# Performance work log

Measured on AMD Instinct MI355X. Metric: run time of the kernel, lower is better.

The kernel has to match this reference:

```python
import jax, jax.numpy as jnp
import numpy as np

D_MODEL = 1024
N_HEADS = 16
D_HEAD = D_MODEL // N_HEADS
BLOCK = 128
B, T = 2, 2048


def setup_inputs() -> dict:
    key = jax.random.key(0)
    ks = jax.random.split(key, 5)
    x = jax.random.normal(ks[0], (B, T, D_MODEL), dtype=jnp.float32)
    def init_w(k):
        # nn.Linear default init scale ~ 1/sqrt(fan_in)
        return jax.random.normal(k, (D_MODEL, D_MODEL), dtype=jnp.float32) / np.sqrt(D_MODEL).astype(np.float32)
    return {
        "x": x,
        "Wq": init_w(ks[1]),
        "Wk": init_w(ks[2]),
        "Wv": init_w(ks[3]),
        "Wo": init_w(ks[4]),
    }


def _flash_attention(Q, K, V, block_size, scale):
    """Online-softmax tiled attention over kv blocks (causal). Q,K,V: (B,H,T,d)."""
    Bb, H, Tt, d = Q.shape
    n_blocks = Tt // block_size
    # (n_blocks, B, H, block, d) so scan streams kv tiles
    Kb = K.reshape(Bb, H, n_blocks, block_size, d).transpose(2, 0, 1, 3, 4)
    Vb = V.reshape(Bb, H, n_blocks, block_size, d).transpose(2, 0, 1, 3, 4)
    starts = jnp.arange(n_blocks) * block_size
    q_pos = jnp.arange(Tt)

    def step(carry, xs):
        m, l, acc = carry
        kb, vb, st = xs
        # scores: (B,H,T,block)
        scores = scale * jnp.einsum('bhtd,bhsd->bhts', Q, kb)
        kv_pos = st + jnp.arange(block_size)
        future = kv_pos[None, :] > q_pos[:, None]          # (T, block)
        scores = jnp.where(future[None, None], -jnp.inf, scores)
        m_new = jnp.maximum(m, jnp.max(scores, axis=-1, keepdims=True))
        p = jnp.exp(scores - m_new)
        corr = jnp.exp(m - m_new)
        l = corr * l + jnp.sum(p, axis=-1, keepdims=True)
        acc = corr * acc + jnp.einsum('bhts,bhsd->bhtd', p, vb)
        return (m_new, l, acc), None

    m0 = jnp.full((Bb, H, Tt, 1), -jnp.inf, dtype=jnp.float32)
    l0 = jnp.zeros((Bb, H, Tt, 1), dtype=jnp.float32)
    a0 = jnp.zeros((Bb, H, Tt, d), dtype=jnp.float32)
    (m, l, acc), _ = jax.lax.scan(step, (m0, l0, a0), (Kb, Vb, starts))
    return acc / jnp.maximum(l, 1e-12)


def reference(x, Wq, Wk, Wv, Wo):
    Bx, Tx, _ = x.shape
    scale = 1.0 / np.sqrt(D_HEAD).astype(np.float32)
    def proj(W):  # nn.Linear: y = x @ W.T
        y = jnp.einsum('btm,nm->btn', x, W)
        return y.reshape(Bx, Tx, N_HEADS, D_HEAD).transpose(0, 2, 1, 3)
    Q, K, V = proj(Wq), proj(Wk), proj(Wv)
    O = _flash_attention(Q.astype(jnp.float32), K.astype(jnp.float32), V.astype(jnp.float32), BLOCK, scale)
    O = O.astype(x.dtype).transpose(0, 2, 1, 3).reshape(Bx, Tx, D_MODEL)
    return jnp.einsum('btm,nm->btn', O, Wo)
```

## Files before the change

kernel.cpp:

```cpp
#include <hip/hip_runtime.h>
#include <hip/hip_bf16.h>

typedef __attribute__((ext_vector_type(8))) short short8;
typedef __attribute__((ext_vector_type(4))) float f32x4;
typedef __attribute__((ext_vector_type(2))) unsigned int uint2v;
typedef __attribute__((ext_vector_type(4))) unsigned int uint4v;
typedef unsigned short u16;

#define MFMA_BF16(a, b, c) __builtin_amdgcn_mfma_f32_16x16x32_bf16(a, b, c, 0, 0, 0)

#define T_SEQ 2048
#define DMODEL 1024
#define NHEADS 16
#define DHEAD 64
#define NEG_BIG (-30000.0f)
#define QSCALE 0.1803368801111f
#define RESCALE_THR 8.0f

#if __has_builtin(__builtin_amdgcn_exp2f)
#define EXP2(x) __builtin_amdgcn_exp2f(x)
#else
#define EXP2(x) exp2f(x)
#endif

__device__ __forceinline__ unsigned bfr(unsigned u) {
  return (u + 0x7fffu + ((u >> 16) & 1u)) >> 16;
}
__device__ __forceinline__ uint4v ld8bf(const float* __restrict__ p) {
  const uint4v a = *(const uint4v*)p;
  const uint4v b = *(const uint4v*)(p + 4);
  uint4v r;
  r[0] = bfr(a[0]) | (bfr(a[1]) << 16);
  r[1] = bfr(a[2]) | (bfr(a[3]) << 16);
  r[2] = bfr(b[0]) | (bfr(b[1]) << 16);
  r[3] = bfr(b[2]) | (bfr(b[3]) << 16);
  return r;
}
__device__ __forceinline__ u16 f2bf(float f) {
  unsigned u = __float_as_uint(f);
  u += 0x7fffu + ((u >> 16) & 1u);
  return (u16)(u >> 16);
}
__device__ __forceinline__ void gld16(const u16* g, u16* l) {
  __builtin_amdgcn_global_load_lds(
      (const __attribute__((address_space(1))) unsigned int*)g,
      (__attribute__((address_space(3))) unsigned int*)l, 16, 0, 0);
}

__global__ __launch_bounds__(256) void cvt_all(
    const float* __restrict__ x, const float* __restrict__ wq,
    const float* __restrict__ wk, const float* __restrict__ wv,
    const float* __restrict__ wo, u16* __restrict__ xh, u16* __restrict__ wqh,
    u16* __restrict__ wkh, u16* __restrict__ wvh, u16* __restrict__ woh) {
  int bi = blockIdx.x;
  const float* s;
  u16* d;
  size_t base;
  if (bi < 2048) {
    s = x; d = xh; base = (size_t)bi * 2048;
  } else {
    int k = (bi - 2048) >> 9;
    int r = (bi - 2048) & 511;
    s = (k == 0) ? wq : (k == 1) ? wk : (k == 2) ? wv : wo;
    d = (k == 0) ? wqh : (k == 1) ? wkh : (k == 2) ? wvh : woh;
    base = (size_t)r * 2048;
  }
  size_t i = base + (size_t)threadIdx.x * 8;
  *(uint4v*)&d[i] = ld8bf(&s[i]);
}

__global__ __launch_bounds__(256) void gemm_qkv(
    const u16* __restrict__ X, const u16* __restrict__ Wq,
    const u16* __restrict__ Wk, const u16* __restrict__ Wv,
    u16* __restrict__ Qo, u16* __restrict__ Ko, u16* __restrict__ Vo) {
  __shared__ __attribute__((aligned(16))) u16 sm[16384];
  const int tid = threadIdx.x, lane = tid & 63, w = tid >> 6;
  const int wm = (w >> 1) * 64, wn = (w & 1) * 64;
  const int lrow = lane & 15;
  const int lk = (lane >> 4) << 3;
  const int lq = (lane >> 4) << 2;

  const int id = blockIdx.x;
  const int xcd = id & 7, r8 = id >> 3;
  const int xo = r8 & 3, yz = r8 >> 2;
  const int y = yz & 7, z = yz >> 3;
  const int mBase = (xcd * 4 + xo) * 128, nBase = y * 128;

  const u16* Bt = (z == 0) ? Wq : (z == 1) ? Wk : Wv;
  u16* D = (z == 0) ? Qo : (z == 1) ? Ko : Vo;
  const float scale = (z == 0) ? QSCALE : 1.0f;

  f32x4 acc[4][4];
#pragma unroll
  for (int mi = 0; mi < 4; mi++)
#pragma unroll
    for (int ni = 0; ni < 4; ni++) acc[mi][ni] = (f32x4)0.0f;

  auto stage = [&](int buf, int k0) {
#pragma unroll
    for (int i = 0; i < 2; i++) {
      int c = i * 256 + tid;
      int r = c >> 2, kk = (c & 3) << 3;
      gld16(&X[(size_t)(mBase + r) * 1024 + k0 + kk], &sm[buf * 4096 + c * 8]);
      gld16(&Bt[(size_t)(nBase + r) * 1024 + k0 + kk],
            &sm[8192 + buf * 4096 + c * 8]);
    }
  };

  stage(0, 0);
  __syncthreads();
  int cur = 0;
  for (int k0 = 0; k0 < 1024; k0 += 32) {
    if (k0 + 32 < 1024) stage(cur ^ 1, k0 + 32);
    short8 af[4], bf[4];
#pragma unroll
    for (int mi = 0; mi < 4; mi++)
      af[mi] = *(const short8*)&sm[cur * 4096 + (wm + mi * 16 + lrow) * 32 + lk];
#pragma unroll
    for (int ni = 0; ni < 4; ni++)
      bf[ni] =
          *(const short8*)&sm[8192 + cur * 4096 + (wn + ni * 16 + lrow) * 32 + lk];
#pragma unroll
    for (int mi = 0; mi < 4; mi++)
#pragma unroll
      for (int ni = 0; ni < 4; ni++)
        acc[mi][ni] = MFMA_BF16(af[mi], bf[ni], acc[mi][ni]);
    __syncthreads();
    cur ^= 1;
  }

  if (z != 2) {
#pragma unroll
    for (int mi = 0; mi < 4; mi++)
#pragma unroll
      for (int r = 0; r < 4; r++) {
        int m = mBase + wm + mi * 16 + lq + r;
        int b = m >> 11, t = m & 2047;
#pragma unroll
        for (int ni = 0; ni < 4; ni++) {
          int n = nBase + wn + ni * 16 + lrow;
          int h = n >> 6, dd = n & 63;
          D[(((size_t)(b * NHEADS + h)) * T_SEQ + t) * DHEAD + dd] =
              f2bf(acc[mi][ni][r] * scale);
        }
      }
  } else {
    u16* TT = &sm[w * 4096];
#pragma unroll
    for (int mi = 0; mi < 4; mi++)
#pragma unroll
      for (int r = 0; r < 4; r++) {
        int t_loc = mi * 16 + lq + r;
#pragma unroll
        for (int ni = 0; ni < 4; ni++) {
          int d_loc = ni * 16 + lrow;
          TT[d_loc * 64 + ((((t_loc >> 3) ^ (d_loc & 7)) << 3) | (t_loc & 7))] =
              f2bf(acc[mi][ni][r]);
        }
      }
    const int b = (mBase + wm) >> 11;
    const int t0 = (mBase + wm) & 2047;
#pragma unroll
    for (int it = 0; it < 8; it++) {
      int d_loc = it * 8 + (lane >> 3);
      int ch = lane & 7;
      short8 v = *(const short8*)&TT[d_loc * 64 + ((ch ^ (d_loc & 7)) << 3)];
      int n = nBase + wn + d_loc;
      int h = n >> 6, dd = n & 63;
      *(uint4v*)&D[(((size_t)((b * NHEADS + h) * DHEAD + dd)) * T_SEQ) + t0 +
                   ch * 8] = *(const uint4v*)&v;
    }
  }
}

__global__ __launch_bounds__(512) void attn_kvsplit(
    const u16* __restrict__ Qg, const u16* __restrict__ Kg,
    const u16* __restrict__ Vtg, u16* __restrict__ Ob) {
  __shared__ __attribute__((aligned(16))) u16 smem[40960];

  const int tid = threadIdx.x;
  const int w = tid >> 6, lane = tid & 63;
  const int g = w >> 2;
  const int wg = w & 3;
  const int lrow = lane & 15;
  const int quad = lane >> 4;
  const int lk = quad << 3;
  const int rsw = lrow & 7;
  const int q_local = wg * 16 + lrow;

  const int id = blockIdx.x;
  const int xcd = id & 7;
  const int r0 = id >> 3;
  const int qt = 31 - (r0 >> 2);
  const int bh = xcd * 4 + (r0 & 3);
  const int b = bh >> 4, h = bh & 15;
  const int qb = qt * 64;
  const u16* Qp = Qg + (size_t)bh * T_SEQ * DHEAD;
  const u16* Kp = Kg + (size_t)bh * T_SEQ * DHEAD;
  const u16* Vp = Vtg + (size_t)bh * DHEAD * T_SEQ;

  auto stage_tile = [&](int T, int p) {
    if (T > qt) return;
    const int slot = (p << 1) | (T & 1);
    const int c = tid;
    const int r = c >> 3;
    const int sw = ((c & 7) ^ (r & 7)) << 3;
    gld16(&Kp[(size_t)(T * 64 + r) * DHEAD + sw],
          &smem[8192 + slot * 4096 + c * 8]);
    gld16(&Vp[(size_t)r * T_SEQ + T * 64 + sw],
          &smem[24576 + slot * 4096 + c * 8]);
  };

  stage_tile(0, 0);
  stage_tile(1, 0);

  short8 qf[2];
#pragma unroll
  for (int ks = 0; ks < 2; ks++)
    qf[ks] = *(const short8*)&Qp[(size_t)(qb + q_local) * DHEAD + ks * 32 + lk];

  float mst = NEG_BIG, lst = 0.f;
  f32x4 oacc[4];
#pragma unroll
  for (int nd = 0; nd < 4; nd++) oacc[nd] = (f32x4)0.0f;
  __syncthreads();

  const int Smax = (qt + 2) >> 1;
  for (int s = 0; s < Smax; s++) {
    const int p = s & 1;
    stage_tile(2 * s + 2, p ^ 1);
    stage_tile(2 * s + 3, p ^ 1);
    const int myt = 2 * s + g;
    if (myt <= qt) {
      const u16* Kc = &smem[8192 + ((p << 1) | g) * 4096];
      const u16* Vc = &smem[24576 + ((p << 1) | g) * 4096];

      f32x4 sv[4];
      __builtin_amdgcn_s_setprio(1);
#pragma unroll
      for (int kvt = 0; kvt < 4; kvt++) {
        f32x4 a = (f32x4)0.0f;
#pragma unroll
        for (int ks = 0; ks < 2; ks++) {
          short8 kf = *(const short8*)&Kc[(kvt * 16 + lrow) * 64 +
                                          ((((ks << 2) + quad) ^ rsw) << 3)];
          a = MFMA_BF16(kf, qf[ks], a);
        }
        sv[kvt] = a;
      }
      __builtin_amdgcn_s_setprio(0);

      if (myt == qt) {
#pragma unroll
        for (int kvt = 0; kvt < 4; kvt++)
#pragma unroll
          for (int r = 0; r < 4; r++)
            if (kvt * 16 + quad * 4 + r > q_local) sv[kvt][r] = NEG_BIG;
      }

      float mx = NEG_BIG;
#pragma unroll
      for (int kvt = 0; kvt < 4; kvt++)
        mx = fmaxf(mx, fmaxf(fmaxf(sv[kvt][0], sv[kvt][1]),
                             fmaxf(sv[kvt][2], sv[kvt][3])));
      mx = fmaxf(mx, __shfl_xor(mx, 16));
      mx = fmaxf(mx, __shfl_xor(mx, 32));
      if (!__all(mx <= mst + RESCALE_THR)) {
        float mn = fmaxf(mst, mx);
        float corr = EXP2(mst - mn);
        mst = mn;
        lst *= corr;
#pragma unroll
        for (int nd = 0; nd < 4; nd++) oacc[nd] *= corr;
      }
      float ls = 0.f;
#pragma unroll
      for (int kvt = 0; kvt < 4; kvt++)
#pragma unroll
        for (int r = 0; r < 4; r++) {
          float pv = EXP2(sv[kvt][r] - mst);
          sv[kvt][r] = pv;
          ls += pv;
        }
      ls += __shfl_xor(ls, 16);
      ls += __shfl_xor(ls, 32);
      lst += ls;

#pragma unroll
      for (int kvt = 0; kvt < 4; kvt++) {
        uint2v pk;
        pk[0] = (__float_as_uint(sv[kvt][0]) >> 16) |
                (__float_as_uint(sv[kvt][1]) & 0xffff0000u);
        pk[1] = (__float_as_uint(sv[kvt][2]) >> 16) |
                (__float_as_uint(sv[kvt][3]) & 0xffff0000u);
        *(uint2v*)&smem[g * 4096 + q_local * 64 +
                        ((((kvt << 1) | (quad >> 1)) ^ rsw) << 3) +
                        ((quad & 1) << 2)] = pk;
      }

      __builtin_amdgcn_s_setprio(1);
#pragma unroll
      for (int ks = 0; ks < 2; ks++) {
        short8 pf = *(const short8*)&smem[g * 4096 + q_local * 64 +
                                          ((((ks << 2) + quad) ^ rsw) << 3)];
#pragma unroll
        for (int nd = 0; nd < 4; nd++) {
          short8 vf = *(const short8*)&Vc[(nd * 16 + lrow) * 64 +
                                          ((((ks << 2) + quad) ^ rsw) << 3)];
          oacc[nd] = MFMA_BF16(vf, pf, oacc[nd]);
        }
      }
      __builtin_amdgcn_s_setprio(0);
    }
    __syncthreads();
  }

  float* O1 = (float*)&smem[8192];
  float* ml = (float*)&smem[24576];
  if (g == 1) {
#pragma unroll
    for (int nd = 0; nd < 4; nd++)
      *(f32x4*)&O1[q_local * 64 + ((((nd << 2) | quad) ^ rsw) << 2)] = oacc[nd];
    if (quad == 0) {
      ml[q_local] = mst;
      ml[64 + q_local] = lst;
    }
  }
  __syncthreads();
  if (g == 0) {
    const float m1 = ml[q_local], l1 = ml[64 + q_local];
    const float M = fmaxf(mst, m1);
    const float c0 = EXP2(mst - M), c1 = EXP2(m1 - M);
    const float inv = 1.f / (c0 * lst + c1 * l1);
    size_t rowbase = ((size_t)(b * T_SEQ + qb + q_local)) * DMODEL + h * DHEAD;
#pragma unroll
    for (int nd = 0; nd < 4; nd++) {
      f32x4 o1 = *(const f32x4*)&O1[q_local * 64 +
                                    ((((nd << 2) | quad) ^ rsw) << 2)];
      uint2v pk;
      pk[0] = (unsigned)f2bf((c0 * oacc[nd][0] + c1 * o1[0]) * inv) |
              ((unsigned)f2bf((c0 * oacc[nd][1] + c1 * o1[1]) * inv) << 16);
      pk[1] = (unsigned)f2bf((c0 * oacc[nd][2] + c1 * o1[2]) * inv) |
              ((unsigned)f2bf((c0 * oacc[nd][3] + c1 * o1[3]) * inv) << 16);
      *(uint2v*)&Ob[rowbase + nd * 16 + quad * 4] = pk;
    }
  }
}

__global__ __launch_bounds__(256) void gemm_out_bf(const u16* __restrict__ O,
                                                   const u16* __restrict__ Wo,
                                                   float* __restrict__ Out) {
  __shared__ __attribute__((aligned(16))) u16 As[2][128 * 32];
  __shared__ __attribute__((aligned(16))) u16 Bs[2][64 * 32];
  const int tid = threadIdx.x, lane = tid & 63, w = tid >> 6;
  const int wm = (w >> 1) * 64, wn = (w & 1) * 32;
  const int lrow = lane & 15;
  const int lk = (lane >> 4) << 3;
  const int lq = (lane >> 4) << 2;

  const int id = blockIdx.x;
  const int xcd = id & 7, r8 = id >> 3;
  const int xo = r8 & 3, y = r8 >> 2;
  const int mBase = (xcd * 4 + xo) * 128, nBase = y * 64;

  f32x4 acc[4][2];
#pragma unroll
  for (int mi = 0; mi < 4; mi++)
#pragma unroll
    for (int ni = 0; ni < 2; ni++) acc[mi][ni] = (f32x4)0.0f;

  auto stage = [&](int buf, int k0) {
#pragma unroll
    for (int i = 0; i < 2; i++) {
      int c = i * 256 + tid;
      int r = c >> 2, kk = (c & 3) << 3;
      gld16(&O[(size_t)(mBase + r) * 1024 + k0 + kk], &As[buf][c * 8]);
    }
    int r = tid >> 2, kk = (tid & 3) << 3;
    gld16(&Wo[(size_t)(nBase + r) * 1024 + k0 + kk], &Bs[buf][tid * 8]);
  };

  stage(0, 0);
  __syncthreads();
  int cur = 0;
  for (int k0 = 0; k0 < 1024; k0 += 32) {
    if (k0 + 32 < 1024) stage(cur ^ 1, k0 + 32);
    short8 af[4], bf[2];
#pragma unroll
    for (int mi = 0; mi < 4; mi++)
      af[mi] = *(const short8*)&As[cur][(wm + mi * 16 + lrow) * 32 + lk];
#pragma unroll
    for (int ni = 0; ni < 2; ni++)
      bf[ni] = *(const short8*)&Bs[cur][(wn + ni * 16 + lrow) * 32 + lk];
#pragma unroll
    for (int mi = 0; mi < 4; mi++)
#pragma unroll
      for (int ni = 0; ni < 2; ni++)
        acc[mi][ni] = MFMA_BF16(af[mi], bf[ni], acc[mi][ni]);
    __syncthreads();
    cur ^= 1;
  }
#pragma unroll
  for (int mi = 0; mi < 4; mi++)
#pragma unroll
    for (int r = 0; r < 4; r++) {
      int m = mBase + wm + mi * 16 + lq + r;
#pragma unroll
      for (int ni = 0; ni < 2; ni++)
        Out[(size_t)m * DMODEL + nBase + wn + ni * 16 + lrow] = acc[mi][ni][r];
    }
}

extern "C" void kernel_launch(void* const* d_in, const int* in_sizes, int n_in,
                              void* d_out, int out_size, void* d_ws,
                              size_t ws_size, hipStream_t stream) {
  const float* x = (const float*)d_in[0];
  const float* Wq = (const float*)d_in[1];
  const float* Wk = (const float*)d_in[2];
  const float* Wv = (const float*)d_in[3];
  const float* Wo = (const float*)d_in[4];
  float* out = (float*)d_out;

  u16* xh = (u16*)d_ws;
  u16* wqh = xh + 4194304;
  u16* wkh = wqh + 1048576;
  u16* wvh = wkh + 1048576;
  u16* woh = wvh + 1048576;
  u16* Q = woh + 1048576;
  u16* K = Q + 4194304;
  u16* V = K + 4194304;
  u16* O = V + 4194304;

  cvt_all<<<dim3(4096), 256, 0, stream>>>(x, Wq, Wk, Wv, Wo, xh, wqh, wkh, wvh, woh);
  gemm_qkv<<<dim3(768), 256, 0, stream>>>(xh, wqh, wkh, wvh, Q, K, V);
  attn_kvsplit<<<dim3(1024), 512, 0, stream>>>(Q, K, V, O);
  gemm_out_bf<<<dim3(512), 256, 0, stream>>>(O, woh, out);
}
```

Before: 175.1 us.

## Rewrite attention with 32x32 MFMA, 128-row query tiles and register P exchange

The attention kernel now uses 32x32x16 bf16 MFMAs, with each wave owning 32 query rows, so a block covers a 128-row query tile and the grid halves to 512 blocks. The P matrix is rearranged into the B-operand layout through cross-lane shuffles instead of a round trip through LDS. The two kv-split groups still alternate tiles from a 4-slot ring, and launch bounds ask for more resident blocks. This should cut LDS traffic and per-MFMA overhead, at the cost of more registers per wave, coarser causal work balance and fewer blocks.

```diff
diff --git a/kernel.cpp b/kernel.cpp
--- a/kernel.cpp
+++ b/kernel.cpp
@@ -3,11 +3,13 @@
 
 typedef __attribute__((ext_vector_type(8))) short short8;
 typedef __attribute__((ext_vector_type(4))) float f32x4;
+typedef __attribute__((ext_vector_type(16))) float f32x16;
 typedef __attribute__((ext_vector_type(2))) unsigned int uint2v;
 typedef __attribute__((ext_vector_type(4))) unsigned int uint4v;
 typedef unsigned short u16;
 
 #define MFMA_BF16(a, b, c) __builtin_amdgcn_mfma_f32_16x16x32_bf16(a, b, c, 0, 0, 0)
+#define MFMA32(a, b, c) __builtin_amdgcn_mfma_f32_32x32x16_bf16(a, b, c, 0, 0, 0)
 
 #define T_SEQ 2048
 #define DMODEL 1024
@@ -40,6 +42,9 @@
   unsigned u = __float_as_uint(f);
   u += 0x7fffu + ((u >> 16) & 1u);
   return (u16)(u >> 16);
+}
+__device__ __forceinline__ unsigned pk2(float a, float b) {
+  return (__float_as_uint(a) >> 16) | (__float_as_uint(b) & 0xffff0000u);
 }
 __device__ __forceinline__ void gld16(const u16* g, u16* l) {
   __builtin_amdgcn_global_load_lds(
@@ -173,97 +178,88 @@
   }
 }
 
-__global__ __launch_bounds__(512) void attn_kvsplit(
+__global__ __launch_bounds__(512, 4) void attn_qt32(
     const u16* __restrict__ Qg, const u16* __restrict__ Kg,
     const u16* __restrict__ Vtg, u16* __restrict__ Ob) {
-  __shared__ __attribute__((aligned(16))) u16 smem[40960];
+  __shared__ __attribute__((aligned(16))) u16 smem[32768];
 
   const int tid = threadIdx.x;
   const int w = tid >> 6, lane = tid & 63;
   const int g = w >> 2;
   const int wg = w & 3;
-  const int lrow = lane & 15;
-  const int quad = lane >> 4;
-  const int lk = quad << 3;
-  const int rsw = lrow & 7;
-  const int q_local = wg * 16 + lrow;
+  const int l31 = lane & 31, h = lane >> 5;
+  const int rsw = l31 & 7;
 
   const int id = blockIdx.x;
-  const int xcd = id & 7;
-  const int r0 = id >> 3;
-  const int qt = 31 - (r0 >> 2);
-  const int bh = xcd * 4 + (r0 & 3);
-  const int b = bh >> 4, h = bh & 15;
-  const int qb = qt * 64;
+  const int half = id >> 8;
+  const int x = id & 255;
+  const int xcd = x & 7;
+  const int u = x >> 3;
+  const int bh = xcd * 4 + (u & 3);
+  const int qp = u >> 2;
+  const int qt = half ? (15 - qp) : qp;
+  const int b = bh >> 4, hh = bh & 15;
+  const int qb = qt << 7;
   const u16* Qp = Qg + (size_t)bh * T_SEQ * DHEAD;
   const u16* Kp = Kg + (size_t)bh * T_SEQ * DHEAD;
   const u16* Vp = Vtg + (size_t)bh * DHEAD * T_SEQ;
-
-  auto stage_tile = [&](int T, int p) {
-    if (T > qt) return;
-    const int slot = (p << 1) | (T & 1);
-    const int c = tid;
-    const int r = c >> 3;
-    const int sw = ((c & 7) ^ (r & 7)) << 3;
-    gld16(&Kp[(size_t)(T * 64 + r) * DHEAD + sw],
-          &smem[8192 + slot * 4096 + c * 8]);
+  const int lastT = 2 * qt + 1;
+
+  auto stage_tile = [&](int T) {
+    if (T > lastT) return;
+    const int slot = T & 3;
+    const int r = tid >> 3;
+    const int sw = ((tid & 7) ^ (r & 7)) << 3;
+    gld16(&Kp[(size_t)(T * 64 + r) * DHEAD + sw], &smem[slot * 4096 + tid * 8]);
     gld16(&Vp[(size_t)r * T_SEQ + T * 64 + sw],
-          &smem[24576 + slot * 4096 + c * 8]);
+          &smem[16384 + slot * 4096 + tid * 8]);
   };
 
-  stage_tile(0, 0);
-  stage_tile(1, 0);
-
-  short8 qf[2];
-#pragma unroll
-  for (int ks = 0; ks < 2; ks++)
-    qf[ks] = *(const short8*)&Qp[(size_t)(qb + q_local) * DHEAD + ks * 32 + lk];
+  stage_tile(0);
+  stage_tile(1);
+
+  const int qg = qb + wg * 32 + l31;
+  short8 qf[4];
+#pragma unroll
+  for (int ks = 0; ks < 4; ks++)
+    qf[ks] = *(const short8*)&Qp[(size_t)qg * DHEAD + ks * 16 + h * 8];
 
   float mst = NEG_BIG, lst = 0.f;
-  f32x4 oacc[4];
-#pragma unroll
-  for (int nd = 0; nd < 4; nd++) oacc[nd] = (f32x4)0.0f;
+  f32x16 oa0 = (f32x16)0.f, oa1 = (f32x16)0.f;
   __syncthreads();
 
-  const int Smax = (qt + 2) >> 1;
-  for (int s = 0; s < Smax; s++) {
-    const int p = s & 1;
-    stage_tile(2 * s + 2, p ^ 1);
-    stage_tile(2 * s + 3, p ^ 1);
-    const int myt = 2 * s + g;
-    if (myt <= qt) {
-      const u16* Kc = &smem[8192 + ((p << 1) | g) * 4096];
-      const u16* Vc = &smem[24576 + ((p << 1) | g) * 4096];
-
-      f32x4 sv[4];
+  for (int s = 0; s <= qt; s++) {
+    stage_tile(2 * s + 2);
+    stage_tile(2 * s + 3);
+    const int T = 2 * s + g;
+    const u16* Kc = &smem[(T & 3) * 4096];
+    const u16* Vc = &smem[16384 + (T & 3) * 4096];
+
+#pragma unroll
+    for (int kvt2 = 0; kvt2 < 2; kvt2++) {
+      f32x16 S = (f32x16)0.f;
       __builtin_amdgcn_s_setprio(1);
 #pragma unroll
-      for (int kvt = 0; kvt < 4; kvt++) {
-        f32x4 a = (f32x4)0.0f;
-#pragma unroll
-        for (int ks = 0; ks < 2; ks++) {
-          short8 kf = *(const short8*)&Kc[(kvt * 16 + lrow) * 64 +
-                                          ((((ks << 2) + quad) ^ rsw) << 3)];
-          a = MFMA_BF16(kf, qf[ks], a);
+      for (int ks = 0; ks < 4; ks++) {
+        short8 kf = *(const short8*)&Kc[(kvt2 * 32 + l31) * 64 +
+                                        (((ks * 2 + h) ^ rsw) << 3)];
+        S = MFMA32(kf, qf[ks], S);
+      }
+      __builtin_amdgcn_s_setprio(0);
+
+      if (s == qt) {
+        const int kvb2 = T * 64 + kvt2 * 32 + 4 * h;
+#pragma unroll
+        for (int r = 0; r < 16; r++) {
+          int kv = kvb2 + (r & 3) + 8 * (r >> 2);
+          if (kv > qg) S[r] = NEG_BIG;
         }
-        sv[kvt] = a;
-      }
-      __builtin_amdgcn_s_setprio(0);
-
-      if (myt == qt) {
-#pragma unroll
-        for (int kvt = 0; kvt < 4; kvt++)
-#pragma unroll
-          for (int r = 0; r < 4; r++)
-            if (kvt * 16 + quad * 4 + r > q_local) sv[kvt][r] = NEG_BIG;
       }
 
       float mx = NEG_BIG;
 #pragma unroll
-      for (int kvt = 0; kvt < 4; kvt++)
-        mx = fmaxf(mx, fmaxf(fmaxf(sv[kvt][0], sv[kvt][1]),
-                             fmaxf(sv[kvt][2], sv[kvt][3])));
-      mx = fmaxf(mx, __shfl_xor(mx, 16));
+      for (int r = 0; r < 16; r += 4)
+        mx = fmaxf(mx, fmaxf(fmaxf(S[r], S[r + 1]), fmaxf(S[r + 2], S[r + 3])));
       mx = fmaxf(mx, __shfl_xor(mx, 32));
       if (!__all(mx <= mst + RESCALE_THR)) {
         float mn = fmaxf(mst, mx);
@@ -271,79 +267,90 @@
         mst = mn;
         lst *= corr;
 #pragma unroll
-        for (int nd = 0; nd < 4; nd++) oacc[nd] *= corr;
+        for (int r = 0; r < 16; r++) {
+          oa0[r] *= corr;
+          oa1[r] *= corr;
+        }
       }
       float ls = 0.f;
 #pragma unroll
-      for (int kvt = 0; kvt < 4; kvt++)
-#pragma unroll
-        for (int r = 0; r < 4; r++) {
-          float pv = EXP2(sv[kvt][r] - mst);
-          sv[kvt][r] = pv;
-          ls += pv;
-        }
-      ls += __shfl_xor(ls, 16);
+      for (int r = 0; r < 16; r++) {
+        float pv = EXP2(S[r] - mst);
+        S[r] = pv;
+        ls += pv;
+      }
       ls += __shfl_xor(ls, 32);
       lst += ls;
 
 #pragma unroll
-      for (int kvt = 0; kvt < 4; kvt++) {
-        uint2v pk;
-        pk[0] = (__float_as_uint(sv[kvt][0]) >> 16) |
-                (__float_as_uint(sv[kvt][1]) & 0xffff0000u);
-        pk[1] = (__float_as_uint(sv[kvt][2]) >> 16) |
-                (__float_as_uint(sv[kvt][3]) & 0xffff0000u);
-        *(uint2v*)&smem[g * 4096 + q_local * 64 +
-                        ((((kvt << 1) | (quad >> 1)) ^ rsw) << 3) +
-                        ((quad & 1) << 2)] = pk;
-      }
-
-      __builtin_amdgcn_s_setprio(1);
-#pragma unroll
-      for (int ks = 0; ks < 2; ks++) {
-        short8 pf = *(const short8*)&smem[g * 4096 + q_local * 64 +
-                                          ((((ks << 2) + quad) ^ rsw) << 3)];
-#pragma unroll
-        for (int nd = 0; nd < 4; nd++) {
-          short8 vf = *(const short8*)&Vc[(nd * 16 + lrow) * 64 +
-                                          ((((ks << 2) + quad) ^ rsw) << 3)];
-          oacc[nd] = MFMA_BF16(vf, pf, oacc[nd]);
-        }
-      }
-      __builtin_amdgcn_s_setprio(0);
+      for (int ks2 = 0; ks2 < 2; ks2++) {
+        unsigned P0 = pk2(S[8 * ks2 + 0], S[8 * ks2 + 1]);
+        unsigned P1 = pk2(S[8 * ks2 + 2], S[8 * ks2 + 3]);
+        unsigned P2 = pk2(S[8 * ks2 + 4], S[8 * ks2 + 5]);
+        unsigned P3 = pk2(S[8 * ks2 + 6], S[8 * ks2 + 7]);
+        unsigned R0 = __shfl_xor(P0, 32), R1 = __shfl_xor(P1, 32);
+        unsigned R2 = __shfl_xor(P2, 32), R3 = __shfl_xor(P3, 32);
+        uint4v fu;
+        fu[0] = h ? R2 : P0;
+        fu[1] = h ? R3 : P1;
+        fu[2] = h ? P2 : R0;
+        fu[3] = h ? P3 : R1;
+        short8 pf = *(short8*)&fu;
+        const int kgr = kvt2 * 4 + ks2 * 2 + h;
+        __builtin_amdgcn_s_setprio(1);
+        short8 vf0 = *(const short8*)&Vc[l31 * 64 + ((kgr ^ rsw) << 3)];
+        oa0 = MFMA32(vf0, pf, oa0);
+        short8 vf1 = *(const short8*)&Vc[(32 + l31) * 64 + ((kgr ^ rsw) << 3)];
+        oa1 = MFMA32(vf1, pf, oa1);
+        __builtin_amdgcn_s_setprio(0);
+      }
     }
     __syncthreads();
   }
 
-  float* O1 = (float*)&smem[8192];
-  float* ml = (float*)&smem[24576];
+  float* O1 = (float*)smem;
+  float* ml = (float*)&smem[16384];
+  const int q = wg * 32 + l31;
   if (g == 1) {
 #pragma unroll
-    for (int nd = 0; nd < 4; nd++)
-      *(f32x4*)&O1[q_local * 64 + ((((nd << 2) | quad) ^ rsw) << 2)] = oacc[nd];
-    if (quad == 0) {
-      ml[q_local] = mst;
-      ml[64 + q_local] = lst;
+    for (int dt = 0; dt < 2; dt++)
+#pragma unroll
+      for (int t4 = 0; t4 < 4; t4++) {
+        int gr = dt * 8 + t4 * 2 + h;
+        int swg = (gr & 8) | ((gr & 7) ^ (q & 7));
+        f32x4 v;
+#pragma unroll
+        for (int j = 0; j < 4; j++) v[j] = dt ? oa1[t4 * 4 + j] : oa0[t4 * 4 + j];
+        *(f32x4*)&O1[q * 64 + swg * 4] = v;
+      }
+    if (h == 0) {
+      ml[q] = mst;
+      ml[128 + q] = lst;
     }
   }
   __syncthreads();
   if (g == 0) {
-    const float m1 = ml[q_local], l1 = ml[64 + q_local];
+    const float m1 = ml[q], l1 = ml[128 + q];
     const float M = fmaxf(mst, m1);
     const float c0 = EXP2(mst - M), c1 = EXP2(m1 - M);
     const float inv = 1.f / (c0 * lst + c1 * l1);
-    size_t rowbase = ((size_t)(b * T_SEQ + qb + q_local)) * DMODEL + h * DHEAD;
-#pragma unroll
-    for (int nd = 0; nd < 4; nd++) {
-      f32x4 o1 = *(const f32x4*)&O1[q_local * 64 +
-                                    ((((nd << 2) | quad) ^ rsw) << 2)];
-      uint2v pk;
-      pk[0] = (unsigned)f2bf((c0 * oacc[nd][0] + c1 * o1[0]) * inv) |
-              ((unsigned)f2bf((c0 * oacc[nd][1] + c1 * o1[1]) * inv) << 16);
-      pk[1] = (unsigned)f2bf((c0 * oacc[nd][2] + c1 * o1[2]) * inv) |
-              ((unsigned)f2bf((c0 * oacc[nd][3] + c1 * o1[3]) * inv) << 16);
-      *(uint2v*)&Ob[rowbase + nd * 16 + quad * 4] = pk;
-    }
+    size_t rowbase = ((size_t)(b * T_SEQ + qb + q)) * DMODEL + hh * DHEAD;
+#pragma unroll
+    for (int dt = 0; dt < 2; dt++)
+#pragma unroll
+      for (int t4 = 0; t4 < 4; t4++) {
+        int gr = dt * 8 + t4 * 2 + h;
+        int swg = (gr & 8) | ((gr & 7) ^ (q & 7));
+        f32x4 o1 = *(const f32x4*)&O1[q * 64 + swg * 4];
+        float a0 = (c0 * (dt ? oa1[t4 * 4 + 0] : oa0[t4 * 4 + 0]) + c1 * o1[0]) * inv;
+        float a1 = (c0 * (dt ? oa1[t4 * 4 + 1] : oa0[t4 * 4 + 1]) + c1 * o1[1]) * inv;
+        float a2 = (c0 * (dt ? oa1[t4 * 4 + 2] : oa0[t4 * 4 + 2]) + c1 * o1[2]) * inv;
+        float a3 = (c0 * (dt ? oa1[t4 * 4 + 3] : oa0[t4 * 4 + 3]) + c1 * o1[3]) * inv;
+        uint2v pk;
+        pk[0] = (unsigned)f2bf(a0) | ((unsigned)f2bf(a1) << 16);
+        pk[1] = (unsigned)f2bf(a2) | ((unsigned)f2bf(a3) << 16);
+        *(uint2v*)&Ob[rowbase + dt * 32 + t4 * 8 + 4 * h] = pk;
+      }
   }
 }
 
@@ -433,6 +440,6 @@
 
   cvt_all<<<dim3(4096), 256, 0, stream>>>(x, Wq, Wk, Wv, Wo, xh, wqh, wkh, wvh, woh);
   gemm_qkv<<<dim3(768), 256, 0, stream>>>(xh, wqh, wkh, wvh, Q, K, V);
-  attn_kvsplit<<<dim3(1024), 512, 0, stream>>>(Q, K, V, O);
+  attn_qt32<<<dim3(512), 512, 0, stream>>>(Q, K, V, O);
   gemm_out_bf<<<dim3(512), 256, 0, stream>>>(O, woh, out);
 }
```

Result: faster. 171.1 us (-2.3%).
